# Kernel optimization log

Measured on AMD Instinct MI355X. Metric: run time of the kernel, lower is better.

Reference implementation:

```python
import jax, jax.numpy as jnp
import numpy as np

N, D, R, DR, H, L = 6000, 128, 1000, 128, 2, 2
MAXN = 1.0 - 4e-3  # Poincare ball projection boundary (c=1)


def _norm(x):
    return jnp.clip(jnp.linalg.norm(x, axis=-1, keepdims=True), 1e-15)


def proj(x):
    n = _norm(x)
    return jnp.where(n > MAXN, x / n * MAXN, x)


def expmap0(u):
    n = _norm(u)
    return proj(jnp.tanh(n) * u / n)


def logmap0(p):
    n = _norm(p)
    return jnp.arctanh(jnp.minimum(n, 1.0 - 1e-7)) * p / n


def mobius_add(x, y):
    x2 = jnp.sum(x * x, -1, keepdims=True)
    y2 = jnp.sum(y * y, -1, keepdims=True)
    xy = jnp.sum(x * y, -1, keepdims=True)
    num = (1 + 2 * xy + y2) * x + (1 - x2) * y
    den = 1 + 2 * xy + x2 * y2
    return num / jnp.clip(den, 1e-15)


def hgc_layer(x, adj, W, b):
    # HypLinear (mobius matvec + hyperbolic bias), HypAgg (tangent-space SpMM), HypAct (relu)
    mv = proj(expmap0(logmap0(x) @ W.T))
    h = proj(mobius_add(mv, proj(expmap0(b))))
    h = proj(expmap0(adj @ logmap0(h)))
    return proj(expmap0(jax.nn.relu(logmap0(h))))


def gat_layer(x, adj, W, a_src, a_dst):
    h = jnp.einsum('nd,hde->hne', x, W)                 # [H,N,D]
    es = jnp.einsum('hne,he->hn', h, a_src)
    ed = jnp.einsum('hne,he->hn', h, a_dst)
    e = jax.nn.leaky_relu(es[:, :, None] + ed[:, None, :], 0.2)  # [H,N,N]
    att = jax.nn.softmax(jnp.where(adj[None] > 0, e, -1e9), axis=-1)
    out = jnp.einsum('hnm,hme->hne', att, h).mean(0)    # head-average -> [N,D]
    return jax.nn.elu(out)


def mha(x, Wq, Wk, Wv, Wfc, g, b):
    # Transformer-style MHA with residual + LayerNorm; x: [N, Lr, D]
    Nn, Lr, _ = x.shape
    split = lambda y: y.reshape(Nn, Lr, H, D).transpose(0, 2, 1, 3)
    q, k, v = split(x @ Wq), split(x @ Wk), split(x @ Wv)
    attn = jax.nn.softmax(jnp.einsum('nhld,nhmd->nhlm', q, k) / jnp.sqrt(jnp.float32(D)), -1)
    o = jnp.einsum('nhlm,nhmd->nhld', attn, v).transpose(0, 2, 1, 3).reshape(Nn, Lr, H * D)
    o = o @ Wfc + x
    mu = o.mean(-1, keepdims=True)
    var = o.var(-1, keepdims=True)
    return g * (o - mu) / jnp.sqrt(var + 1e-6) + b


def _forward(ent_sr, ent_tg, rel_sr, rel_tg, adj_sr, adj_tg, rel_adj_sr, rel_adj_tg,
             gat_W, gat_a_src, gat_a_dst, Wq, Wk, Wv, Wfc, ln_g, ln_b, hgc_W, hgc_b):
    # Relation Aggregator: sparse mm + rowsum normalization
    def rel_agg(radj, remb):
        return (radj @ remb) / radj.sum(-1, keepdims=True)
    sr_rel = rel_agg(rel_adj_sr, rel_sr)
    tg_rel = rel_agg(rel_adj_tg, rel_tg)

    # Attentive Neighbor Aggregator + multi-range fusion (res=True -> range = L+1)
    def branch(x, adj):
        outs, h = [x], x
        for i in range(L):
            h = gat_layer(h, adj, gat_W[i], gat_a_src[i], gat_a_dst[i])
            h = h / jnp.clip(_norm(h), 1e-12)  # F.normalize(dim=1)
            outs.append(h)
        seq = jnp.stack(outs, axis=1)  # [N, L+1, D]
        return mha(seq, Wq, Wk, Wv, Wfc, ln_g, ln_b).mean(1)
    sr = branch(ent_sr, adj_sr)
    tg = branch(ent_tg, adj_tg)

    # Hyperbolic encoder (proj_tan0 is identity for PoincareBall)
    def encode(x, adj):
        h = expmap0(x)
        for i in range(2):
            h = hgc_layer(h, adj, hgc_W[i], hgc_b[i])
        return logmap0(h)
    hs = ent_sr + encode(ent_sr, adj_sr)
    ht = ent_tg + encode(ent_tg, adj_tg)

    return (jnp.concatenate([sr, sr_rel], -1), jnp.concatenate([tg, tg_rel], -1),
            jnp.concatenate([hs, sr_rel], -1), jnp.concatenate([ht, tg_rel], -1))


def setup_inputs() -> dict:
    key = jax.random.key(0)
    ks = jax.random.split(key, 24)

    def make_adj(k):
        m = jax.random.bernoulli(k, 32.0 / N, (N, N)) | jnp.eye(N, dtype=bool)
        a = m.astype(jnp.float32)
        return a / a.sum(-1, keepdims=True)

    def make_rel_adj(k1, k2):
        m = jax.random.bernoulli(k1, 5.0 / R, (N, R)).astype(jnp.float32)
        idx = jax.random.randint(k2, (N,), 0, R)
        return m.at[jnp.arange(N), idx].set(1.0)  # guarantee positive rowsum

    return {
        'ent_sr': 0.02 * jax.random.normal(ks[0], (N, D)),
        'ent_tg': 0.02 * jax.random.normal(ks[1], (N, D)),
        'rel_sr': 0.02 * jax.random.normal(ks[2], (R, DR)),
        'rel_tg': 0.02 * jax.random.normal(ks[3], (R, DR)),
        'adj_sr': make_adj(ks[4]),
        'adj_tg': make_adj(ks[5]),
        'rel_adj_sr': make_rel_adj(ks[6], ks[7]),
        'rel_adj_tg': make_rel_adj(ks[8], ks[9]),
        'gat_W': 0.1 * jax.random.normal(ks[10], (L, H, D, D)),
        'gat_a_src': 0.1 * jax.random.normal(ks[11], (L, H, D)),
        'gat_a_dst': 0.1 * jax.random.normal(ks[12], (L, H, D)),
        'Wq': 0.05 * jax.random.normal(ks[13], (D, H * D)),
        'Wk': 0.05 * jax.random.normal(ks[14], (D, H * D)),
        'Wv': 0.05 * jax.random.normal(ks[15], (D, H * D)),
        'Wfc': 0.05 * jax.random.normal(ks[16], (H * D, D)),
        'ln_g': jnp.ones((D,)),
        'ln_b': jnp.zeros((D,)),
        'hgc_W': 0.05 * jax.random.normal(ks[17], (2, D, D)),
        'hgc_b': 0.01 * jax.random.normal(ks[18], (2, D)),
    }


def reference(ent_sr, ent_tg, rel_sr, rel_tg, adj_sr, adj_tg, rel_adj_sr, rel_adj_tg,
              gat_W, gat_a_src, gat_a_dst, Wq, Wk, Wv, Wfc, ln_g, ln_b, hgc_W, hgc_b):
    return _forward(ent_sr, ent_tg, rel_sr, rel_tg, adj_sr, adj_tg, rel_adj_sr, rel_adj_tg,
                    gat_W, gat_a_src, gat_a_dst, Wq, Wk, Wv, Wfc, ln_g, ln_b, hgc_W, hgc_b)
```

## Files before the change

### kernel.cpp

```cpp
#include <hip/hip_runtime.h>
#include <hip/hip_bf16.h>
#include <math.h>

#define NN   6000
#define N2   12000
#define DD   128
#define RR   1000
#define CAP  96
#define CAPR 48
#define MAXN_F 0.996f

typedef short  bf16x8 __attribute__((ext_vector_type(8)));
typedef float  f32x4  __attribute__((ext_vector_type(4)));
typedef unsigned u32x4 __attribute__((ext_vector_type(4)));

__device__ int      g_dt[19];
__device__ unsigned g_csri[N2 * CAP];
__device__ int      g_cnt[N2];
__device__ float    g_seq[N2 * 3 * DD];
__device__ unsigned short g_seqb[3 * N2 * DD];
__device__ unsigned short g_hhb[N2 * 256];
__device__ float    g_es[2][N2];
__device__ float    g_ed[2][N2];
__device__ unsigned short g_zy[(size_t)N2 * 3 * 512];
__device__ float    g_t[N2 * DD];
__device__ float    g_t2[N2 * DD];
__device__ unsigned short g_WgatT[2][256 * DD];
__device__ unsigned short g_WzyT[512 * DD];
__device__ float    g_WhgcT[2][DD * DD];

__device__ __forceinline__ float ldin(const void* p, size_t i, int bf) {
    if (bf) return __uint_as_float(((unsigned)((const unsigned short*)p)[i]) << 16);
    return ((const float*)p)[i];
}
__device__ __forceinline__ unsigned short f2b(float f) {
    unsigned u = __float_as_uint(f);
    u += 0x7FFFu + ((u >> 16) & 1u);
    return (unsigned short)(u >> 16);
}
__device__ __forceinline__ float b2f(unsigned short b) {
    return __uint_as_float(((unsigned)b) << 16);
}
__device__ __forceinline__ float adjval(int c) {
    return b2f(f2b(1.0f / (float)c));
}

__device__ __forceinline__ float wsum(float v) {
    #pragma unroll
    for (int o = 32; o > 0; o >>= 1) v += __shfl_xor(v, o, 64);
    return v;
}
__device__ __forceinline__ float wmax(float v) {
    #pragma unroll
    for (int o = 32; o > 0; o >>= 1) v = fmaxf(v, __shfl_xor(v, o, 64));
    return v;
}

struct P19 { const void* p[19]; };

__global__ void detect_all(P19 ptrs) {
    const int sizes[19] = {768000,768000,128000,128000,36000000,36000000,6000000,6000000,
                           65536,512,512,32768,32768,32768,32768,128,128,32768,256};
    __shared__ int votes[2];
    if (threadIdx.x == 0) { votes[0] = 0; votes[1] = 0; }
    __syncthreads();
    int slot = blockIdx.x < 19 ? blockIdx.x : 17;
    const unsigned* p = (const unsigned*)ptrs.p[slot];
    int nwords = sizes[slot] / 2;
    if (nwords > 0) {
        int nsamp = nwords < 4096 ? nwords : 4096;
        int stride = nwords / nsamp; if (stride < 1) stride = 1;
        for (int s = threadIdx.x; s < nsamp; s += blockDim.x) {
            unsigned lo = p[(size_t)s * stride] & 0xFFFFu;
            if (lo) {
                unsigned e = (lo >> 7) & 0xFFu;
                if (e >= 100u && e <= 140u) atomicAdd(&votes[1], 1);
                else                        atomicAdd(&votes[0], 1);
            }
        }
    }
    __syncthreads();
    int isbf = (votes[1] > votes[0]) ? 1 : 0;
    if (blockIdx.x < 19) {
        if (threadIdx.x == 0) g_dt[blockIdx.x] = isbf;
    } else {
        for (int i = threadIdx.x; i < 32768; i += blockDim.x) {
            int j = i & 127, d = (i >> 7) & 127, l = i >> 14;
            g_WhgcT[l][j * 128 + d] = ldin(ptrs.p[17], i, isbf);
        }
    }
}

__global__ __launch_bounds__(128) void compose_zy(P19 in) {
    int c = blockIdx.x;
    int i = threadIdx.x;
    int matsel = c >> 8;
    int h = (c >> 7) & 1, oo = c & 127;
    int slotA = matsel ? 13 : 11;
    int slotB = matsel ? 14 : 12;
    const void* A = in.p[slotA];
    const void* B = in.p[slotB];
    const int bfA = g_dt[slotA], bfB = g_dt[slotB];
    __shared__ float bvec[128];
    if (matsel == 0) bvec[i] = ldin(B, (size_t)oo * 256 + h * 128 + i, bfB);
    else             bvec[i] = ldin(B, (size_t)(h * 128 + i) * 128 + oo, bfB);
    __syncthreads();
    float acc = 0.f;
    #pragma unroll 16
    for (int e = 0; e < 128; e++)
        acc = fmaf(ldin(A, (size_t)i * 256 + h * 128 + e, bfA), bvec[e], acc);
    g_WzyT[(size_t)c * 128 + i] = f2b(acc);
}

__device__ __forceinline__ void bias_wave(const void* hgc_b, int layer, int lane,
                                          float& y0, float& y1, float& y2) {
    float b0 = ldin(hgc_b, (size_t)layer * DD + lane, g_dt[18]);
    float b1 = ldin(hgc_b, (size_t)layer * DD + 64 + lane, g_dt[18]);
    float ss = wsum(b0 * b0 + b1 * b1);
    float nrm = fmaxf(sqrtf(ss), 1e-15f);
    float t = tanhf(nrm);
    float s = t / nrm;
    float vn = t;
    if (t > MAXN_F) { s *= MAXN_F / t; vn = MAXN_F; }
    y0 = s * b0; y1 = s * b1;
    y2 = vn * vn;
}

__device__ __forceinline__ void hgc_lin_w(const float* uw, int layer, int lane,
                                          float y0, float y1, float y2,
                                          float& o0, float& o1) {
    const float* W = g_WhgcT[layer];
    float mv0 = 0.f, mv1 = 0.f;
    #pragma unroll 16
    for (int j = 0; j < DD; j++) {
        float uj = uw[j];
        mv0 = fmaf(W[j * 128 + lane], uj, mv0);
        mv1 = fmaf(W[j * 128 + 64 + lane], uj, mv1);
    }
    float ss2 = wsum(mv0 * mv0 + mv1 * mv1);
    float nm = fmaxf(sqrtf(ss2), 1e-15f);
    float t2 = tanhf(nm);
    float sc = t2 / nm; float xn = t2;
    if (t2 > MAXN_F) { sc *= MAXN_F / t2; xn = MAXN_F; }
    float x0 = sc * mv0, x1 = sc * mv1;
    float x2 = xn * xn;
    float xy = wsum(x0 * y0 + x1 * y1);
    float a = 1.f + 2.f * xy + y2;
    float den = 1.f + 2.f * xy + x2 * y2;
    den = (fabsf(den) < 1e-15f) ? 1e-15f : den;
    float h0 = (a * x0 + (1.f - x2) * y0) / den;
    float h1 = (a * x1 + (1.f - x2) * y1) / den;
    float s3 = wsum(h0 * h0 + h1 * h1);
    float nn = fmaxf(sqrtf(s3), 1e-15f);
    float f = 1.f;
    if (nn > MAXN_F) { f = MAXN_F / nn; nn = MAXN_F; }
    float lg = atanhf(fminf(nn, 1.f - 1e-7f)) / nn;
    o0 = lg * f * h0; o1 = lg * f * h1;
}

__device__ __forceinline__ void hgc_agg_w(const float* tin, int n, int which, int lane,
                                          unsigned* bas, float& o0, float& o1) {
    int c = min(g_cnt[n], CAP);
    const unsigned* idx = &g_csri[(size_t)n * CAP];
    if (lane < c)      bas[lane]      = (idx[lane]      + (unsigned)(which * NN)) * 128u;
    if (64 + lane < c) bas[64 + lane] = (idx[64 + lane] + (unsigned)(which * NN)) * 128u;
    float a0 = 0.f, a1 = 0.f;
    int j = 0;
    for (; j + 4 <= c; j += 4) {
        unsigned b0 = bas[j], b1 = bas[j + 1], b2 = bas[j + 2], b3 = bas[j + 3];
        float v0 = tin[(size_t)b0 + lane], v1 = tin[(size_t)b1 + lane];
        float v2 = tin[(size_t)b2 + lane], v3 = tin[(size_t)b3 + lane];
        float w0 = tin[(size_t)b0 + 64 + lane], w1 = tin[(size_t)b1 + 64 + lane];
        float w2 = tin[(size_t)b2 + 64 + lane], w3 = tin[(size_t)b3 + 64 + lane];
        a0 += (v0 + v1) + (v2 + v3);
        a1 += (w0 + w1) + (w2 + w3);
    }
    for (; j < c; j++) {
        unsigned bb = bas[j];
        a0 += tin[(size_t)bb + lane];
        a1 += tin[(size_t)bb + 64 + lane];
    }
    float sc = (c > 0) ? adjval(c) : 0.f;
    a0 *= sc; a1 *= sc;
    float ss = wsum(a0 * a0 + a1 * a1);
    float nm = fmaxf(sqrtf(ss), 1e-15f);
    float t = tanhf(nm);
    float s1 = t / nm; float xn = t;
    if (t > MAXN_F) { s1 *= MAXN_F / t; xn = MAXN_F; }
    float lg = atanhf(fminf(xn, 1.f - 1e-7f)) / fmaxf(xn, 1e-15f);
    float u0 = fmaxf(lg * s1 * a0, 0.f), u1 = fmaxf(lg * s1 * a1, 0.f);
    float ss2 = wsum(u0 * u0 + u1 * u1);
    float nm2 = fmaxf(sqrtf(ss2), 1e-15f);
    float t2 = tanhf(nm2);
    float s2 = t2 / nm2; float xn2 = t2;
    if (t2 > MAXN_F) { s2 *= MAXN_F / t2; xn2 = MAXN_F; }
    float lg2 = atanhf(fminf(xn2, 1.f - 1e-7f)) / fmaxf(xn2, 1e-15f);
    o0 = lg2 * s2 * u0; o1 = lg2 * s2 * u1;
}

__global__ __launch_bounds__(256) void front_mega(P19 in, float* __restrict__ out) {
    int b = blockIdx.x;
    int tid = threadIdx.x;
    int w = tid >> 6, lane = tid & 63;
    int phase, pb;
    if (b < 9000) { pb = b / 3; phase = b - pb * 3; }
    else { phase = 3; pb = b - 9000; }

    if (phase == 0) {
        int which = pb >= 1500 ? 1 : 0;
        int row = ((which ? pb - 1500 : pb) << 2) | w;
        const void* A = in.p[4 + which];
        int gn = which * NN + row;
        __shared__ int cnt4[4];
        if (lane == 0) cnt4[w] = 0;
        __syncthreads();
        unsigned* dst = &g_csri[(size_t)gn * CAP];
        if (g_dt[4 + which]) {
            const u32x4* p = (const u32x4*)((const unsigned short*)A + (size_t)row * NN);
            #pragma unroll
            for (int c0 = 0; c0 < 12; c0 += 6) {
                u32x4 v[6];
                #pragma unroll
                for (int u = 0; u < 6; u++) {
                    int idx = (c0 + u) * 64 + lane;
                    if (idx < 750) v[u] = __builtin_nontemporal_load(&p[idx]);
                    else v[u] = (u32x4)(0u);
                }
                #pragma unroll
                for (int u = 0; u < 6; u++) {
                    int idx = (c0 + u) * 64 + lane;
                    #pragma unroll
                    for (int h = 0; h < 4; h++) {
                        unsigned w32 = v[u][h];
                        if (w32) {
                            unsigned lo = w32 & 0xFFFFu, hi = w32 >> 16;
                            if (lo && !(lo & 0x8000u)) {
                                int q = atomicAdd(&cnt4[w], 1);
                                if (q < CAP) dst[q] = (unsigned)(idx * 8 + h * 2);
                            }
                            if (hi && !(hi & 0x8000u)) {
                                int q = atomicAdd(&cnt4[w], 1);
                                if (q < CAP) dst[q] = (unsigned)(idx * 8 + h * 2 + 1);
                            }
                        }
                    }
                }
            }
        } else {
            const f32x4* p = (const f32x4*)((const float*)A + (size_t)row * NN);
            #pragma unroll
            for (int c0 = 0; c0 < 24; c0 += 6) {
                f32x4 v[6];
                #pragma unroll
                for (int u = 0; u < 6; u++) {
                    int idx = (c0 + u) * 64 + lane;
                    if (idx < 1500) v[u] = __builtin_nontemporal_load(&p[idx]);
                    else v[u] = (f32x4)(0.f);
                }
                #pragma unroll
                for (int u = 0; u < 6; u++) {
                    int idx = (c0 + u) * 64 + lane;
                    #pragma unroll
                    for (int h = 0; h < 4; h++) {
                        if (v[u][h] > 0.f) {
                            int q = atomicAdd(&cnt4[w], 1);
                            if (q < CAP) dst[q] = (unsigned)(idx * 4 + h);
                        }
                    }
                }
            }
        }
        __syncthreads();
        if (lane == 0) g_cnt[gn] = min(cnt4[w], CAP);
    } else if (phase == 1) {
        int n = pb * 4 + w;
        int which = n >= NN ? 1 : 0;
        int row = n - which * NN;
        const void* radj = in.p[6 + which];
        const void* rel  = in.p[2 + which];
        const int bfa = g_dt[6 + which], bfr = g_dt[2 + which];
        __shared__ int rl_list[4][CAPR];
        __shared__ int rl_cs[4];
        if (lane == 0) rl_cs[w] = 0;
        if (bfa) {
            const uint4* p = (const uint4*)((const unsigned short*)radj + (size_t)row * RR);
            #pragma unroll
            for (int rep = 0; rep < 2; rep++) {
                int i = rep * 64 + lane;
                if (i < 125) {
                    uint4 w4 = p[i];
                    unsigned ws4[4] = {w4.x, w4.y, w4.z, w4.w};
                    #pragma unroll
                    for (int h = 0; h < 4; h++) {
                        unsigned lo = ws4[h] & 0xFFFFu, hi = ws4[h] >> 16;
                        if (lo && !(lo & 0x8000u)) { int q = atomicAdd(&rl_cs[w], 1); if (q < CAPR) rl_list[w][q] = i * 8 + h * 2; }
                        if (hi && !(hi & 0x8000u)) { int q = atomicAdd(&rl_cs[w], 1); if (q < CAPR) rl_list[w][q] = i * 8 + h * 2 + 1; }
                    }
                }
            }
        } else {
            const float4* p = (const float4*)((const float*)radj + (size_t)row * RR);
            #pragma unroll
            for (int rep = 0; rep < 4; rep++) {
                int i = rep * 64 + lane;
                if (i < 250) {
                    float4 w4 = p[i];
                    float vs[4] = {w4.x, w4.y, w4.z, w4.w};
                    #pragma unroll
                    for (int h = 0; h < 4; h++)
                        if (vs[h] > 0.f) { int q = atomicAdd(&rl_cs[w], 1); if (q < CAPR) rl_list[w][q] = i * 4 + h; }
                }
            }
        }
        int c = min(rl_cs[w], CAPR);
        float a0 = 0.f, a1 = 0.f;
        for (int j = 0; j < c; j++) {
            int li = rl_list[w][j];
            a0 += ldin(rel, (size_t)li * DD + lane, bfr);
            a1 += ldin(rel, (size_t)li * DD + 64 + lane, bfr);
        }
        float r0 = c ? a0 / (float)c : 0.f;
        float r1 = c ? a1 / (float)c : 0.f;
        out[(size_t)n * 256 + 128 + lane] = r0;
        out[(size_t)n * 256 + 192 + lane] = r1;
        out[(size_t)(2 * NN + n) * 256 + 128 + lane] = r0;
        out[(size_t)(2 * NN + n) * 256 + 192 + lane] = r1;
    } else if (phase == 2) {
        int n = pb * 4 + w;
        int which = n >= NN ? 1 : 0;
        int row = n - which * NN;
        __shared__ float us[4][128];
        float y0, y1, y2v;
        bias_wave(in.p[18], 0, lane, y0, y1, y2v);
        float x0 = ldin(in.p[which], (size_t)row * DD + lane, g_dt[which]);
        float x1 = ldin(in.p[which], (size_t)row * DD + 64 + lane, g_dt[which]);
        g_seq[(size_t)n * 384 + lane] = x0;
        g_seq[(size_t)n * 384 + 64 + lane] = x1;
        g_seqb[(size_t)n * DD + lane] = f2b(x0);
        g_seqb[(size_t)n * DD + 64 + lane] = f2b(x1);
        float ss = wsum(x0 * x0 + x1 * x1);
        float nrm = fmaxf(sqrtf(ss), 1e-15f);
        float t = tanhf(nrm);
        float scale = t / nrm;
        float hn = t;
        if (t > MAXN_F) { scale *= MAXN_F / t; hn = MAXN_F; }
        float lgx = atanhf(fminf(hn, 1.f - 1e-7f)) / fmaxf(hn, 1e-15f);
        us[w][lane] = lgx * scale * x0;
        us[w][64 + lane] = lgx * scale * x1;
        float o0, o1;
        hgc_lin_w(us[w], 0, lane, y0, y1, y2v, o0, o1);
        g_t[(size_t)n * DD + lane] = o0;
        g_t[(size_t)n * DD + 64 + lane] = o1;
    } else {
        int stride = 128 * 256;
        int base = pb * 256 + tid;
        const int b8 = g_dt[8];
        for (int i = base; i < 65536; i += stride) {
            int e = i & 127, d = (i >> 7) & 127, h = (i >> 14) & 1, l = (i >> 15) & 1;
            g_WgatT[l][(h * 128 + e) * DD + d] = f2b(ldin(in.p[8], i, b8));
        }
    }
}

__global__ __launch_bounds__(256) void gemm_scores(P19 in, int layer, float* __restrict__ out) {
    int tid = threadIdx.x;
    int w = tid >> 6, lane = tid & 63;
    if (blockIdx.x >= 750) {
        int n = (blockIdx.x - 750) * 4 + w;
        int which = n >= NN ? 1 : 0;
        __shared__ unsigned bas[4][CAP];
        if (layer == 0) {
            __shared__ float us[4][128];
            float y0, y1, y2v;
            bias_wave(in.p[18], 1, lane, y0, y1, y2v);
            float u0, u1;
            hgc_agg_w(g_t, n, which, lane, bas[w], u0, u1);
            us[w][lane] = u0; us[w][64 + lane] = u1;
            float o0, o1;
            hgc_lin_w(us[w], 1, lane, y0, y1, y2v, o0, o1);
            g_t2[(size_t)n * DD + lane] = o0;
            g_t2[(size_t)n * DD + 64 + lane] = o1;
        } else {
            float u0, u1;
            hgc_agg_w(g_t2, n, which, lane, bas[w], u0, u1);
            float ev0 = ldin(which ? in.p[1] : in.p[0], (size_t)(n - which * NN) * DD + lane, g_dt[which]);
            float ev1 = ldin(which ? in.p[1] : in.p[0], (size_t)(n - which * NN) * DD + 64 + lane, g_dt[which]);
            out[(size_t)(2 * NN + n) * 256 + lane]      = ev0 + u0;
            out[(size_t)(2 * NN + n) * 256 + 64 + lane] = ev1 + u1;
        }
        return;
    }
    int q = lane >> 4, ln = lane & 15;
    int bm = blockIdx.x * 16;
    const unsigned short* A = g_seqb + (size_t)layer * (N2 * DD);
    const unsigned short* Bt = g_WgatT[layer];
    int colbase = w * 64;
    f32x4 acc[4] = {};
    #pragma unroll
    for (int s = 0; s < 4; s++) {
        int kc = s * 4 + q;
        bf16x8 af = *(const bf16x8*)(A + (size_t)(bm + ln) * DD + kc * 8);
        #pragma unroll
        for (int nt = 0; nt < 4; nt++) {
            bf16x8 bf = *(const bf16x8*)(Bt + (size_t)(colbase + nt * 16 + ln) * DD + kc * 8);
            acc[nt] = __builtin_amdgcn_mfma_f32_16x16x32_bf16(af, bf, acc[nt], 0, 0, 0);
        }
    }
    #pragma unroll
    for (int nt = 0; nt < 4; nt++) {
        int col = colbase + nt * 16 + ln;
        #pragma unroll
        for (int r = 0; r < 4; r++) {
            int row = bm + q * 4 + r;
            g_hhb[(size_t)row * 256 + col] = f2b(acc[nt][r]);
        }
    }
    const int bfs = g_dt[9], bfd = g_dt[10];
    float a_s[4], a_d[4];
    #pragma unroll
    for (int nt = 0; nt < 4; nt++) {
        int col = colbase + nt * 16 + ln;
        size_t ab = ((size_t)layer * 2 + (col >> 7)) * DD + (col & 127);
        a_s[nt] = ldin(in.p[9],  ab, bfs);
        a_d[nt] = ldin(in.p[10], ab, bfd);
    }
    __shared__ float pS[4][16], pD[4][16];
    #pragma unroll
    for (int r = 0; r < 4; r++) {
        float ps = 0.f, pd = 0.f;
        #pragma unroll
        for (int nt = 0; nt < 4; nt++) {
            ps = fmaf(acc[nt][r], a_s[nt], ps);
            pd = fmaf(acc[nt][r], a_d[nt], pd);
        }
        #pragma unroll
        for (int o = 1; o < 16; o <<= 1) {
            ps += __shfl_xor(ps, o, 64);
            pd += __shfl_xor(pd, o, 64);
        }
        if (ln == 0) { pS[w][q * 4 + r] = ps; pD[w][q * 4 + r] = pd; }
    }
    __syncthreads();
    if (tid < 16) {
        g_es[0][bm + tid] = pS[0][tid] + pS[1][tid];
        g_es[1][bm + tid] = pS[2][tid] + pS[3][tid];
        g_ed[0][bm + tid] = pD[0][tid] + pD[1][tid];
        g_ed[1][bm + tid] = pD[2][tid] + pD[3][tid];
    }
}

__global__ __launch_bounds__(256) void gemm_zy() {
    __shared__ __align__(16) unsigned short As[16 * 128 * 8];
    __shared__ __align__(16) unsigned short Bs[16 * 128 * 8];
    int bm = blockIdx.y * 128, bn = blockIdx.x * 128;
    int tid = threadIdx.x;
    int lane = tid & 63, w = tid >> 6;
    int q = lane >> 4, ln = lane & 15;
    const int M = N2 * 3;
    f32x4 acc[8][2] = {};
    #pragma unroll
    for (int i = 0; i < 8; i++) {
        int combo = w * 8 + i;
        int c = combo >> 1, half = combo & 1;
        int r = half * 64 + lane;
        int gm = bm + r; if (gm >= M) gm = M - 1;
        int n = gm / 3, l = gm - n * 3;
        *(uint4*)&As[(c * 128 + r) * 8] =
            *(const uint4*)(g_seqb + (size_t)l * (N2 * DD) + (size_t)n * DD + c * 8);
        *(uint4*)&Bs[(c * 128 + r) * 8] =
            *(const uint4*)(g_WzyT + (size_t)(bn + r) * DD + c * 8);
    }
    __syncthreads();
    #pragma unroll
    for (int s = 0; s < 4; s++) {
        bf16x8 bf0 = *(const bf16x8*)&Bs[((s * 4 + q) * 128 + w * 32 + ln) * 8];
        bf16x8 bf1 = *(const bf16x8*)&Bs[((s * 4 + q) * 128 + w * 32 + 16 + ln) * 8];
        #pragma unroll
        for (int mt = 0; mt < 8; mt++) {
            bf16x8 af = *(const bf16x8*)&As[((s * 4 + q) * 128 + mt * 16 + ln) * 8];
            acc[mt][0] = __builtin_amdgcn_mfma_f32_16x16x32_bf16(af, bf0, acc[mt][0], 0, 0, 0);
            acc[mt][1] = __builtin_amdgcn_mfma_f32_16x16x32_bf16(af, bf1, acc[mt][1], 0, 0, 0);
        }
    }
    #pragma unroll
    for (int mt = 0; mt < 8; mt++) {
        #pragma unroll
        for (int nt = 0; nt < 2; nt++) {
            int gcol = bn + w * 32 + nt * 16 + ln;
            #pragma unroll
            for (int r = 0; r < 4; r++) {
                int grow = bm + mt * 16 + q * 4 + r;
                if (grow < M)
                    g_zy[(size_t)grow * 512 + gcol] = f2b(acc[mt][nt][r]);
            }
        }
    }
}

__global__ __launch_bounds__(256) void gat_attn(int layer) {
    int tid = threadIdx.x;
    int w = tid >> 6, lane = tid & 63;
    int n = blockIdx.x * 4 + w;
    int which = n >= NN ? 1 : 0;
    int c = min(g_cnt[n], CAP);
    __shared__ unsigned bas[4][CAP];
    __shared__ float w0s[4][CAP], w1s[4][CAP];
    float es0 = g_es[0][n], es1 = g_es[1][n];
    float e0a = -1e30f, e1a = -1e30f, e0b = -1e30f, e1b = -1e30f;
    if (lane < c) {
        int gI = (int)g_csri[(size_t)n * CAP + lane] + which * NN;
        bas[w][lane] = (unsigned)gI * 128u;
        e0a = es0 + g_ed[0][gI]; e0a = e0a > 0.f ? e0a : 0.2f * e0a;
        e1a = es1 + g_ed[1][gI]; e1a = e1a > 0.f ? e1a : 0.2f * e1a;
    }
    if (64 + lane < c) {
        int gI = (int)g_csri[(size_t)n * CAP + 64 + lane] + which * NN;
        bas[w][64 + lane] = (unsigned)gI * 128u;
        e0b = es0 + g_ed[0][gI]; e0b = e0b > 0.f ? e0b : 0.2f * e0b;
        e1b = es1 + g_ed[1][gI]; e1b = e1b > 0.f ? e1b : 0.2f * e1b;
    }
    float m0 = wmax(fmaxf(e0a, e0b));
    float m1 = wmax(fmaxf(e1a, e1b));
    float x0a = (lane < c) ? expf(e0a - m0) : 0.f;
    float x1a = (lane < c) ? expf(e1a - m1) : 0.f;
    float x0b = (64 + lane < c) ? expf(e0b - m0) : 0.f;
    float x1b = (64 + lane < c) ? expf(e1b - m1) : 0.f;
    float s0 = wsum(x0a + x0b), s1 = wsum(x1a + x1b);
    float r0 = 1.f / fmaxf(s0, 1e-30f), r1 = 1.f / fmaxf(s1, 1e-30f);
    if (lane < c)      { w0s[w][lane] = x0a * r0;      w1s[w][lane] = x1a * r1; }
    if (64 + lane < c) { w0s[w][64 + lane] = x0b * r0; w1s[w][64 + lane] = x1b * r1; }
    const unsigned* hh32 = (const unsigned*)g_hhb;
    float aLe = 0.f, aLo = 0.f, aHe = 0.f, aHo = 0.f;
    #pragma unroll 4
    for (int j = 0; j < c; j++) {
        unsigned bb = bas[w][j];
        unsigned vlo = hh32[(size_t)bb + lane];
        unsigned vhi = hh32[(size_t)bb + 64 + lane];
        float g0 = w0s[w][j], g1 = w1s[w][j];
        aLe = fmaf(g0, b2f((unsigned short)(vlo & 0xFFFFu)), aLe);
        aLo = fmaf(g0, b2f((unsigned short)(vlo >> 16)), aLo);
        aHe = fmaf(g1, b2f((unsigned short)(vhi & 0xFFFFu)), aHe);
        aHo = fmaf(g1, b2f((unsigned short)(vhi >> 16)), aHo);
    }
    float o0 = (c > 0) ? 0.5f * (aLe + aHe) : 0.f;
    float o1 = (c > 0) ? 0.5f * (aLo + aHo) : 0.f;
    o0 = o0 > 0.f ? o0 : expm1f(o0);
    o1 = o1 > 0.f ? o1 : expm1f(o1);
    float ss = wsum(o0 * o0 + o1 * o1);
    float rn = 1.f / fmaxf(sqrtf(ss), 1e-12f);
    o0 *= rn; o1 *= rn;
    g_seq[(size_t)n * 384 + (layer + 1) * 128 + 2 * lane] = o0;
    g_seq[(size_t)n * 384 + (layer + 1) * 128 + 2 * lane + 1] = o1;
    size_t pbase = (size_t)(layer + 1) * (N2 * DD) + (size_t)n * DD + 2 * lane;
    *(unsigned*)&g_seqb[pbase] = (unsigned)f2b(o0) | ((unsigned)f2b(o1) << 16);
}

__global__ __launch_bounds__(256) void mha_out(const void* __restrict__ g,
                                               const void* __restrict__ bb_,
                                               float* __restrict__ out) {
    int tid = threadIdx.x;
    int w = tid >> 6, lane = tid & 63;
    int n = blockIdx.x * 4 + w;
    int dl = 2 * lane;
    float xm[3][2], zf[3][2][2];
    #pragma unroll
    for (int l = 0; l < 3; l++) {
        unsigned xv = *(const unsigned*)(g_seqb + (size_t)l * (N2 * DD) + (size_t)n * DD + dl);
        xm[l][0] = b2f((unsigned short)(xv & 0xFFFFu));
        xm[l][1] = b2f((unsigned short)(xv >> 16));
        size_t zb = (size_t)(n * 3 + l) * 512;
        #pragma unroll
        for (int h = 0; h < 2; h++) {
            unsigned zv = *(const unsigned*)(g_zy + zb + h * 128 + dl);
            zf[l][h][0] = b2f((unsigned short)(zv & 0xFFFFu));
            zf[l][h][1] = b2f((unsigned short)(zv >> 16));
        }
    }
    float att[2][3][3];
    #pragma unroll
    for (int h = 0; h < 2; h++)
        #pragma unroll
        for (int l = 0; l < 3; l++)
            #pragma unroll
            for (int m = 0; m < 3; m++) {
                float p = zf[l][h][0] * xm[m][0] + zf[l][h][1] * xm[m][1];
                #pragma unroll
                for (int o = 32; o > 0; o >>= 1) p += __shfl_xor(p, o, 64);
                att[h][l][m] = p * 0.08838834764831845f;
            }
    #pragma unroll
    for (int h = 0; h < 2; h++)
        #pragma unroll
        for (int l = 0; l < 3; l++) {
            float mx = fmaxf(att[h][l][0], fmaxf(att[h][l][1], att[h][l][2]));
            float ea = expf(att[h][l][0] - mx), eb = expf(att[h][l][1] - mx),
                  ec = expf(att[h][l][2] - mx);
            float s = 1.f / fmaxf(ea + eb + ec, 1e-30f);
            att[h][l][0] = ea * s; att[h][l][1] = eb * s; att[h][l][2] = ec * s;
        }
    float yv[3][2][2];
    #pragma unroll
    for (int m = 0; m < 3; m++) {
        size_t yb = (size_t)(n * 3 + m) * 512 + 256;
        #pragma unroll
        for (int h = 0; h < 2; h++) {
            unsigned v = *(const unsigned*)(g_zy + yb + h * 128 + dl);
            yv[m][h][0] = b2f((unsigned short)(v & 0xFFFFu));
            yv[m][h][1] = b2f((unsigned short)(v >> 16));
        }
    }
    float ool[3][2], mu[3], rstd[3];
    #pragma unroll
    for (int l = 0; l < 3; l++) {
        float f0 = 0.f, f1 = 0.f;
        #pragma unroll
        for (int h = 0; h < 2; h++)
            #pragma unroll
            for (int m = 0; m < 3; m++) {
                f0 = fmaf(att[h][l][m], yv[m][h][0], f0);
                f1 = fmaf(att[h][l][m], yv[m][h][1], f1);
            }
        const float* sq = g_seq + (size_t)n * 384 + l * 128 + dl;
        ool[l][0] = f0 + sq[0];
        ool[l][1] = f1 + sq[1];
    }
    #pragma unroll
    for (int l = 0; l < 3; l++) {
        float s  = wsum(ool[l][0] + ool[l][1]);
        float ss = wsum(ool[l][0] * ool[l][0] + ool[l][1] * ool[l][1]);
        mu[l] = s / 128.f;
        rstd[l] = rsqrtf(ss / 128.f - mu[l] * mu[l] + 1e-6f);
    }
    float acc0 = 0.f, acc1 = 0.f;
    #pragma unroll
    for (int l = 0; l < 3; l++) {
        acc0 += (ool[l][0] - mu[l]) * rstd[l];
        acc1 += (ool[l][1] - mu[l]) * rstd[l];
    }
    const int bg = g_dt[15], bb = g_dt[16];
    out[(size_t)n * 256 + dl]     = ldin(g, dl, bg) * (acc0 / 3.f) + ldin(bb_, dl, bb);
    out[(size_t)n * 256 + dl + 1] = ldin(g, dl + 1, bg) * (acc1 / 3.f) + ldin(bb_, dl + 1, bb);
}

extern "C" void kernel_launch(void* const* d_in, const int* in_sizes, int n_in,
                              void* d_out, int out_size, void* d_ws, size_t ws_size,
                              hipStream_t stream) {
    const void* ln_g = d_in[15];
    const void* ln_b = d_in[16];

    float* out = (float*)d_out;

    P19 ptrs;
    for (int i = 0; i < 19; i++) ptrs.p[i] = d_in[i];
    detect_all<<<20, 1024, 0, stream>>>(ptrs);
    compose_zy<<<512, 128, 0, stream>>>(ptrs);

    front_mega<<<9128, 256, 0, stream>>>(ptrs, out);

    gemm_scores<<<3750, 256, 0, stream>>>(ptrs, 0, out);
    gat_attn<<<3000, 256, 0, stream>>>(0);
    gemm_scores<<<3750, 256, 0, stream>>>(ptrs, 1, out);
    gat_attn<<<3000, 256, 0, stream>>>(1);

    gemm_zy<<<dim3(4, 282), 256, 0, stream>>>();
    mha_out<<<3000, 256, 0, stream>>>(ln_g, ln_b, out);
}
```

Measured before the change: 580.9 us.

## Split zy GEMM per plane and fuse planes into gemm_scores launches

Replaces the single batched zy GEMM with a per-plane register-only MFMA routine that reads operands straight from global memory without LDS staging. Planes 0 and 1 are computed by extra blocks appended to the two gemm_scores launches, so that work overlaps with the score and HGC computation. Plane 2 runs alone in a smaller kernel. The aim is to fill idle GPU capacity in the earlier launches and shorten the tail GEMM, at the cost of redundant B-tile global loads per block and less reuse than the shared-memory tiled version.

New measurement: 597.4 us. 1.03x slower.

```diff
diff --git a/kernel.cpp b/kernel.cpp
--- a/kernel.cpp
+++ b/kernel.cpp
@@ -196,6 +196,35 @@
     if (t2 > MAXN_F) { s2 *= MAXN_F / t2; xn2 = MAXN_F; }
     float lg2 = atanhf(fminf(xn2, 1.f - 1e-7f)) / fmaxf(xn2, 1e-15f);
     o0 = lg2 * s2 * u0; o1 = lg2 * s2 * u1;
+}
+
+__device__ __forceinline__ void zy_plane(int l, int tile, int tid) {
+    int w = tid >> 6, lane = tid & 63;
+    int q = lane >> 4, ln = lane & 15;
+    int bx = tile & 1, by = tile >> 1;
+    int bm = by * 16, bn = bx * 256;
+    const unsigned short* A = g_seqb + (size_t)l * (N2 * DD);
+    int colbase = bn + w * 64;
+    f32x4 acc[4] = {};
+    #pragma unroll
+    for (int s = 0; s < 4; s++) {
+        int kc = s * 4 + q;
+        bf16x8 af = *(const bf16x8*)(A + (size_t)(bm + ln) * DD + kc * 8);
+        #pragma unroll
+        for (int nt = 0; nt < 4; nt++) {
+            bf16x8 bf = *(const bf16x8*)(g_WzyT + (size_t)(colbase + nt * 16 + ln) * DD + kc * 8);
+            acc[nt] = __builtin_amdgcn_mfma_f32_16x16x32_bf16(af, bf, acc[nt], 0, 0, 0);
+        }
+    }
+    #pragma unroll
+    for (int nt = 0; nt < 4; nt++) {
+        int col = colbase + nt * 16 + ln;
+        #pragma unroll
+        for (int r = 0; r < 4; r++) {
+            int n = bm + q * 4 + r;
+            g_zy[(size_t)(n * 3 + l) * 512 + col] = f2b(acc[nt][r]);
+        }
+    }
 }
 
 __global__ __launch_bounds__(256) void front_mega(P19 in, float* __restrict__ out) {
@@ -365,6 +394,10 @@
 __global__ __launch_bounds__(256) void gemm_scores(P19 in, int layer, float* __restrict__ out) {
     int tid = threadIdx.x;
     int w = tid >> 6, lane = tid & 63;
+    if (blockIdx.x >= 3750) {
+        zy_plane(layer, blockIdx.x - 3750, tid);
+        return;
+    }
     if (blockIdx.x >= 750) {
         int n = (blockIdx.x - 750) * 4 + w;
         int which = n >= NN ? 1 : 0;
@@ -449,52 +482,8 @@
     }
 }
 
-__global__ __launch_bounds__(256) void gemm_zy() {
-    __shared__ __align__(16) unsigned short As[16 * 128 * 8];
-    __shared__ __align__(16) unsigned short Bs[16 * 128 * 8];
-    int bm = blockIdx.y * 128, bn = blockIdx.x * 128;
-    int tid = threadIdx.x;
-    int lane = tid & 63, w = tid >> 6;
-    int q = lane >> 4, ln = lane & 15;
-    const int M = N2 * 3;
-    f32x4 acc[8][2] = {};
-    #pragma unroll
-    for (int i = 0; i < 8; i++) {
-        int combo = w * 8 + i;
-        int c = combo >> 1, half = combo & 1;
-        int r = half * 64 + lane;
-        int gm = bm + r; if (gm >= M) gm = M - 1;
-        int n = gm / 3, l = gm - n * 3;
-        *(uint4*)&As[(c * 128 + r) * 8] =
-            *(const uint4*)(g_seqb + (size_t)l * (N2 * DD) + (size_t)n * DD + c * 8);
-        *(uint4*)&Bs[(c * 128 + r) * 8] =
-            *(const uint4*)(g_WzyT + (size_t)(bn + r) * DD + c * 8);
-    }
-    __syncthreads();
-    #pragma unroll
-    for (int s = 0; s < 4; s++) {
-        bf16x8 bf0 = *(const bf16x8*)&Bs[((s * 4 + q) * 128 + w * 32 + ln) * 8];
-        bf16x8 bf1 = *(const bf16x8*)&Bs[((s * 4 + q) * 128 + w * 32 + 16 + ln) * 8];
-        #pragma unroll
-        for (int mt = 0; mt < 8; mt++) {
-            bf16x8 af = *(const bf16x8*)&As[((s * 4 + q) * 128 + mt * 16 + ln) * 8];
-            acc[mt][0] = __builtin_amdgcn_mfma_f32_16x16x32_bf16(af, bf0, acc[mt][0], 0, 0, 0);
-            acc[mt][1] = __builtin_amdgcn_mfma_f32_16x16x32_bf16(af, bf1, acc[mt][1], 0, 0, 0);
-        }
-    }
-    #pragma unroll
-    for (int mt = 0; mt < 8; mt++) {
-        #pragma unroll
-        for (int nt = 0; nt < 2; nt++) {
-            int gcol = bn + w * 32 + nt * 16 + ln;
-            #pragma unroll
-            for (int r = 0; r < 4; r++) {
-                int grow = bm + mt * 16 + q * 4 + r;
-                if (grow < M)
-                    g_zy[(size_t)grow * 512 + gcol] = f2b(acc[mt][nt][r]);
-            }
-        }
-    }
+__global__ __launch_bounds__(256) void gemm_zy_p2() {
+    zy_plane(2, blockIdx.x, threadIdx.x);
 }
 
 __global__ __launch_bounds__(256) void gat_attn(int layer) {
@@ -657,11 +646,11 @@
 
     front_mega<<<9128, 256, 0, stream>>>(ptrs, out);
 
-    gemm_scores<<<3750, 256, 0, stream>>>(ptrs, 0, out);
+    gemm_scores<<<5250, 256, 0, stream>>>(ptrs, 0, out);
     gat_attn<<<3000, 256, 0, stream>>>(0);
-    gemm_scores<<<3750, 256, 0, stream>>>(ptrs, 1, out);
+    gemm_scores<<<5250, 256, 0, stream>>>(ptrs, 1, out);
     gat_attn<<<3000, 256, 0, stream>>>(1);
 
-    gemm_zy<<<dim3(4, 282), 256, 0, stream>>>();
+    gemm_zy_p2<<<1500, 256, 0, stream>>>();
     mha_out<<<3000, 256, 0, stream>>>(ln_g, ln_b, out);
 }
```
